# Kernel tuning notes

Hardware: AMD Instinct MI355X
Metric: run time of the kernel (lower is better)

Reference implementation:

```python
import jax, jax.numpy as jnp
import numpy as np

D_MODEL = 1024
NUM_HEADS = 16
HEAD_DIM = D_MODEL // NUM_HEADS
THETA = 10000.0
B, S = 2, 2048


def _apply_rope(t, cos, sin):
    # t: [B, H, S, hd]; cos/sin: [S, hd//2]
    te = t[..., 0::2]
    to = t[..., 1::2]
    re = te * cos - to * sin
    ro = te * sin + to * cos
    out = jnp.stack([re, ro], axis=-1)  # [B,H,S,hd//2,2]
    return out.reshape(t.shape)


def setup_inputs() -> dict:
    key = jax.random.key(0)
    kx, kq, kk, kv, ko = jax.random.split(key, 5)
    std = 2.0 / (2 * D_MODEL) ** 0.5
    def w(k):
        return jnp.clip(std * jax.random.normal(k, (D_MODEL, D_MODEL), jnp.float32), -3.0 * std, 3.0 * std)
    return {
        "x": jax.random.normal(kx, (B, S, D_MODEL), jnp.float32),
        "Wq": w(kq),
        "Wk": w(kk),
        "Wv": w(kv),
        "Wo": w(ko),
    }


def reference(x, Wq, Wk, Wv, Wo):
    Bv, Sv, _ = x.shape
    def proj(W):
        return jnp.einsum('bsd,ed->bse', x, W).reshape(Bv, Sv, NUM_HEADS, HEAD_DIM).transpose(0, 2, 1, 3)
    q, k, v = proj(Wq), proj(Wk), proj(Wv)

    pos = jnp.arange(Sv, dtype=jnp.float32)
    inv_freq = THETA ** (-jnp.arange(0, HEAD_DIM, 2, dtype=jnp.float32) / HEAD_DIM)
    ang = pos[:, None] * inv_freq[None, :]  # [S, hd//2]
    cos, sin = jnp.cos(ang), jnp.sin(ang)
    q = _apply_rope(q, cos, sin)
    k = _apply_rope(k, cos, sin)

    scale = 1.0 / jnp.sqrt(jnp.float32(HEAD_DIM))
    scores = jnp.einsum('bhqd,bhkd->bhqk', q.astype(jnp.float32), k.astype(jnp.float32)) * scale
    causal = jnp.tril(jnp.ones((Sv, Sv), dtype=bool))
    scores = jnp.where(causal[None, None], scores, -jnp.inf)
    attn = jax.nn.softmax(scores, axis=-1)
    out = jnp.einsum('bhqk,bhkd->bhqd', attn, v.astype(jnp.float32))
    out = out.transpose(0, 2, 1, 3).reshape(Bv, Sv, D_MODEL)
    return jnp.einsum('bsd,ed->bse', out, Wo)
```

## Files before the change

### kernel.cpp

```cpp
#include <hip/hip_runtime.h>
#include <hip/hip_bf16.h>
#include <stdint.h>

typedef __bf16 bf16x8 __attribute__((ext_vector_type(8)));
typedef float  f32x4  __attribute__((ext_vector_type(4)));

__device__ __forceinline__ float bf2f(unsigned short u) {
    union { float f; uint32_t i; } v; v.i = ((uint32_t)u) << 16; return v.f;
}
__device__ __forceinline__ unsigned short f2bf(float f) {
    union { float f; uint32_t i; } v; v.f = f;
    uint32_t r = v.i + 0x7FFF + ((v.i >> 16) & 1);
    return (unsigned short)(r >> 16);
}
__device__ __forceinline__ unsigned short f2bf_rz(float f) {
    union { float f; uint32_t i; } v; v.f = f;
    return (unsigned short)(v.i >> 16);
}

#define GLD_LDS(gptr, lptr) \
    __builtin_amdgcn_global_load_lds( \
        (const __attribute__((address_space(1))) void*)(gptr), \
        (__attribute__((address_space(3))) void*)(lptr), 16, 0, 0)

__global__ __launch_bounds__(256) void convert_inputs(
    const void* __restrict__ x,  const void* __restrict__ wq,
    const void* __restrict__ wk, const void* __restrict__ wv,
    const void* __restrict__ wo, unsigned short* __restrict__ dst,
    unsigned short* __restrict__ wob_dst, int* __restrict__ flag)
{
    __shared__ int cnt[256];
    const int tid = threadIdx.x;
    uint32_t u = ((const uint32_t*)x)[tid];
    int e = (u >> 7) & 0xFF;
    cnt[tid] = (e >= 100 && e <= 140) ? 1 : 0;
    __syncthreads();
    for (int s = 128; s > 0; s >>= 1) {
        if (tid < s) cnt[tid] += cnt[tid + s];
        __syncthreads();
    }
    const int isf32 = (cnt[0] >= 128) ? 0 : 1;
    if (blockIdx.x == 0 && tid == 0) flag[0] = isf32 ? 0 : 1;

    int c = blockIdx.x * 256 + tid;
    const void* src; size_t off; unsigned short* out;
    if (c < 524288)      { src = x;  off = (size_t)c * 8;            out = dst + (size_t)c * 8; }
    else if (c < 655360) { src = wq; off = (size_t)(c - 524288) * 8; out = dst + (size_t)c * 8; }
    else if (c < 786432) { src = wk; off = (size_t)(c - 655360) * 8; out = dst + (size_t)c * 8; }
    else if (c < 917504) { src = wv; off = (size_t)(c - 786432) * 8; out = dst + (size_t)c * 8; }
    else                 { src = wo; off = (size_t)(c - 917504) * 8; out = wob_dst + off; }
    unsigned short t[8];
    if (isf32) {
        const float* s = (const float*)src + off;
        float4 f0 = *(const float4*)s;
        float4 f1 = *(const float4*)(s + 4);
        t[0] = f2bf(f0.x); t[1] = f2bf(f0.y); t[2] = f2bf(f0.z); t[3] = f2bf(f0.w);
        t[4] = f2bf(f1.x); t[5] = f2bf(f1.y); t[6] = f2bf(f1.z); t[7] = f2bf(f1.w);
    } else {
        *(uint4*)t = *(const uint4*)((const unsigned short*)src + off);
    }
    *(uint4*)out = *(const uint4*)t;
}

__global__ __launch_bounds__(512, 2) void gemm_qkv_8ph(
    const unsigned short* __restrict__ A,
    const unsigned short* __restrict__ B0,
    const unsigned short* __restrict__ B1,
    const unsigned short* __restrict__ B2,
    unsigned short* __restrict__ O0,
    unsigned short* __restrict__ O1,
    unsigned short* __restrict__ O2)
{
    __shared__ __align__(16) unsigned short Asl[2][16384];
    __shared__ __align__(16) unsigned short Bsl[2][16384];

    const int tid  = threadIdx.x;
    const int lane = tid & 63;
    const int wid  = tid >> 6;
    const int wm   = wid >> 2;
    const int wn   = wid & 3;
    const int lr   = lane & 15;
    const int quad = lane >> 4;

    const int m0  = blockIdx.y * 256;
    const int n0g = blockIdx.x * 256;
    const int sel = n0g >> 10;
    const unsigned short* Bp = (sel == 0) ? B0 : ((sel == 1) ? B1 : B2);
    unsigned short* Optr     = (sel == 0) ? O0 : ((sel == 1) ? O1 : O2);
    const int n0  = n0g & 1023;

    const int sw0 = ((0 + quad) ^ (lr & 7)) * 8;
    const int sw1 = ((4 + quad) ^ (lr & 7)) * 8;

    f32x4 acc[2][4][2][2] = {};
    bf16x8 aF[4][2];
    bf16x8 bF[2][2];

#define STAGEA(T, H) do { \
    const int tA_ = (T); \
    _Pragma("unroll") \
    for (int p_ = 0; p_ < 2; ++p_) { \
        int c_   = p_ * 512 + tid; \
        int row_ = c_ >> 3; \
        int sc_  = ((c_ & 7) ^ (row_ & 7)) * 8; \
        GLD_LDS(&A[(size_t)(m0 + (H) * 128 + row_) * 1024 + tA_ * 64 + sc_], \
                &Asl[tA_ & 1][(H) * 8192 + c_ * 8]); \
    } } while (0)

#define STAGEB(T, H) do { \
    const int tB_ = (T); \
    _Pragma("unroll") \
    for (int p_ = 0; p_ < 2; ++p_) { \
        int c_   = p_ * 512 + tid; \
        int row_ = c_ >> 3; \
        int sc_  = ((c_ & 7) ^ (row_ & 7)) * 8; \
        GLD_LDS(&Bp[(size_t)(n0 + (H) * 128 + row_) * 1024 + tB_ * 64 + sc_], \
                &Bsl[tB_ & 1][(H) * 8192 + c_ * 8]); \
    } } while (0)

#define LOADA(BUF, QM) do { \
    _Pragma("unroll") \
    for (int fm_ = 0; fm_ < 4; ++fm_) { \
        const int row_ = (QM) * 128 + wm * 64 + fm_ * 16 + lr; \
        aF[fm_][0] = *(const bf16x8*)&Asl[BUF][row_ * 64 + sw0]; \
        aF[fm_][1] = *(const bf16x8*)&Asl[BUF][row_ * 64 + sw1]; \
    } } while (0)

#define LOADB(BUF, QN) do { \
    _Pragma("unroll") \
    for (int fn_ = 0; fn_ < 2; ++fn_) { \
        const int row_ = (QN) * 128 + wn * 32 + fn_ * 16 + lr; \
        bF[fn_][0] = *(const bf16x8*)&Bsl[BUF][row_ * 64 + sw0]; \
        bF[fn_][1] = *(const bf16x8*)&Bsl[BUF][row_ * 64 + sw1]; \
    } } while (0)

#define MFMA16(QM, QN) do { \
    __builtin_amdgcn_s_setprio(1); \
    _Pragma("unroll") \
    for (int fm_ = 0; fm_ < 4; ++fm_) { \
        _Pragma("unroll") \
        for (int fn_ = 0; fn_ < 2; ++fn_) { \
            acc[QM][fm_][QN][fn_] = __builtin_amdgcn_mfma_f32_16x16x32_bf16( \
                aF[fm_][0], bF[fn_][0], acc[QM][fm_][QN][fn_], 0, 0, 0); \
            acc[QM][fm_][QN][fn_] = __builtin_amdgcn_mfma_f32_16x16x32_bf16( \
                aF[fm_][1], bF[fn_][1], acc[QM][fm_][QN][fn_], 0, 0, 0); \
        } \
    } \
    __builtin_amdgcn_s_setprio(0); \
    } while (0)

#define BARRIER() __builtin_amdgcn_s_barrier()
#define LGKM0()   asm volatile("s_waitcnt lgkmcnt(0)" ::: "memory")

    STAGEB(0, 0);
    STAGEA(0, 1);
    STAGEA(0, 0);
    STAGEB(0, 1);
    STAGEB(1, 0);
    STAGEA(1, 1);
    asm volatile("s_waitcnt vmcnt(4)" ::: "memory");
    BARRIER();

    const int NT = 16;
#pragma unroll 2
    for (int t = 0; t < NT; ++t) {
        const int buf = t & 1;

        LOADA(buf, 0);
        LOADB(buf, 0);
        if (t + 1 < NT) STAGEA(t + 1, 0);
        BARRIER();
        LGKM0();
        MFMA16(0, 0);
        BARRIER();

        LOADA(buf, 1);
        if (t + 1 < NT) STAGEB(t + 1, 1);
        BARRIER();
        LGKM0();
        MFMA16(1, 0);
        BARRIER();

        LOADB(buf, 1);
        if (t + 2 < NT) STAGEB(t + 2, 0);
        BARRIER();
        LGKM0();
        MFMA16(1, 1);
        BARRIER();

        LOADA(buf, 0);
        if (t + 2 < NT) STAGEA(t + 2, 1);
        BARRIER();
        LGKM0();
        MFMA16(0, 1);
        if (t + 2 < NT) asm volatile("s_waitcnt vmcnt(4)" ::: "memory");
        else            asm volatile("s_waitcnt vmcnt(0)" ::: "memory");
        BARRIER();
    }

#pragma unroll
    for (int qm = 0; qm < 2; ++qm) {
#pragma unroll
        for (int fm = 0; fm < 4; ++fm) {
            const int mb = m0 + qm * 128 + wm * 64 + fm * 16 + quad * 4;
#pragma unroll
            for (int qn = 0; qn < 2; ++qn) {
#pragma unroll
                for (int fn = 0; fn < 2; ++fn) {
                    const int nl = n0 + qn * 128 + wn * 32 + fn * 16 + lr;
                    const int h = nl >> 6, d = nl & 63;
#pragma unroll
                    for (int r = 0; r < 4; ++r) {
                        const int m = mb + r;
                        const int b = m >> 11, s = m & 2047;
                        Optr[((size_t)(b * 16 + h) * 2048 + s) * 64 + d] =
                            f2bf(acc[qm][fm][qn][fn][r]);
                    }
                }
            }
        }
    }
#undef STAGEA
#undef STAGEB
#undef LOADA
#undef LOADB
#undef MFMA16
#undef BARRIER
#undef LGKM0
}

__global__ __launch_bounds__(256) void gemm_out(
    const unsigned short* __restrict__ P0,
    const unsigned short* __restrict__ P1,
    const float* __restrict__ Lsum,
    const unsigned short* __restrict__ B0,
    void* __restrict__ O,
    const int* __restrict__ flag)
{
    const int K = 1024;
    __shared__ __align__(16) unsigned short As[64 * 64];
    __shared__ __align__(16) unsigned short Bs[128 * 64];

    const int isf32 = (flag[0] == 0) ? 1 : 0;

    const int tid  = threadIdx.x;
    const int lane = tid & 63;
    const int wid  = tid >> 6;
    const int wm   = wid >> 1;
    const int wn   = wid & 1;
    const int lr   = lane & 15;
    const int quad = lane >> 4;
    const int q8   = quad * 8;

    const int m0 = blockIdx.y * 64;
    const int n0 = blockIdx.x * 128;

    f32x4 acc[2][4] = {};

    for (int kk = 0; kk < K; kk += 64) {
        __syncthreads();
        const int h = kk >> 6;
        for (int p = 0; p < 2; ++p) {
            int c   = p * 256 + tid;
            int row = c >> 3;
            int d0  = (c & 7) * 8;
            int m   = m0 + row;
            int b   = m >> 11, s = m & 2047;
            int li  = (b * 16 + h) * 2048 + s;
            float inv = 1.0f / (Lsum[li] + Lsum[65536 + li]);
            size_t addr = ((size_t)li) * 64 + d0;
            unsigned short a[8], bb[8], o[8];
            *(uint4*)a  = *(const uint4*)&P0[addr];
            *(uint4*)bb = *(const uint4*)&P1[addr];
            for (int j = 0; j < 8; ++j)
                o[j] = f2bf((bf2f(a[j]) + bf2f(bb[j])) * inv);
            *(uint4*)&As[c * 8] = *(const uint4*)o;
        }
        for (int p = 0; p < 4; ++p) {
            int c   = p * 256 + tid;
            int row = c >> 3;
            int c8  = (c & 7) * 8;
            GLD_LDS(&B0[(size_t)(n0 + row) * K + kk + c8], &Bs[c * 8]);
        }
        __syncthreads();

        for (int ks = 0; ks < 64; ks += 32) {
            bf16x8 af[2], bf[4];
            for (int t = 0; t < 2; ++t)
                af[t] = *(const bf16x8*)&As[(wm * 32 + t * 16 + lr) * 64 + ks + q8];
            for (int t = 0; t < 4; ++t)
                bf[t] = *(const bf16x8*)&Bs[(wn * 64 + t * 16 + lr) * 64 + ks + q8];
            for (int mt = 0; mt < 2; ++mt)
                for (int nt = 0; nt < 4; ++nt)
                    acc[mt][nt] = __builtin_amdgcn_mfma_f32_16x16x32_bf16(
                        af[mt], bf[nt], acc[mt][nt], 0, 0, 0);
        }
    }

    for (int mt = 0; mt < 2; ++mt) {
        for (int nt = 0; nt < 4; ++nt) {
            for (int r = 0; r < 4; ++r) {
                int m  = m0 + wm * 32 + mt * 16 + quad * 4 + r;
                int nl = n0 + wn * 64 + nt * 16 + lr;
                float val = acc[mt][nt][r];
                if (isf32) ((float*)O)[(size_t)m * 1024 + nl] = val;
                else ((unsigned short*)O)[(size_t)m * 1024 + nl] = f2bf(val);
            }
        }
    }
}

__global__ __launch_bounds__(256) void rope_transpose(
    unsigned short* __restrict__ Q, unsigned short* __restrict__ Kp,
    const unsigned short* __restrict__ V, unsigned short* __restrict__ Vt)
{
    __shared__ unsigned short T[64 * 65];
    const int tid = threadIdx.x;

    if (blockIdx.x < 4096) {
        const int CH = 32 * 2048 * 8;
        int idx = blockIdx.x * 256 + tid;
        bool isK = idx >= CH;
        int j = isK ? (idx - CH) : idx;
        unsigned short* p = isK ? Kp : Q;

        int c8   = j & 7;
        int srow = j >> 3;
        int s    = srow & 2047;
        int off  = srow * 64 + c8 * 8;

        uint4 raw = *(const uint4*)&p[off];
        unsigned short t[8];
        *(uint4*)t = raw;
        float sf = (float)s;
        float qs = isK ? 1.0f : 0.125f;
        for (int jj = 0; jj < 4; ++jj) {
            int i = c8 * 4 + jj;
            float inv = __expf(-0.2878231366f * (float)i);
            float ang = sf * inv;
            float sn = __sinf(ang);
            float cs = __cosf(ang);
            float e = bf2f(t[2 * jj]);
            float o = bf2f(t[2 * jj + 1]);
            t[2 * jj]     = f2bf((e * cs - o * sn) * qs);
            t[2 * jj + 1] = f2bf((e * sn + o * cs) * qs);
        }
        *(uint4*)&p[off] = *(const uint4*)t;
    } else {
        int bidx = blockIdx.x - 4096;
        const int s0 = (bidx & 31) * 64;
        const int bh = bidx >> 5;

        const unsigned short* src = V + ((size_t)bh * 2048 + s0) * 64;
        for (int p = 0; p < 2; ++p) {
            int c = p * 256 + tid;
            int s  = c >> 3;
            int d8 = (c & 7) * 8;
            uint4 raw = *(const uint4*)&src[s * 64 + d8];
            unsigned short t[8];
            *(uint4*)t = raw;
            for (int j = 0; j < 8; ++j) T[s * 65 + d8 + j] = t[j];
        }
        __syncthreads();
        unsigned short* dst = Vt + (size_t)bh * 64 * 2048 + s0;
        for (int p = 0; p < 2; ++p) {
            int c = p * 256 + tid;
            int d  = c >> 3;
            int s8 = (c & 7) * 8;
            unsigned short t[8];
            for (int j = 0; j < 8; ++j) t[j] = T[(s8 + j) * 65 + d];
            *(uint4*)&dst[(size_t)d * 2048 + s8] = *(const uint4*)t;
        }
    }
}

__global__ __launch_bounds__(256) void attn_kernel(
    const unsigned short* __restrict__ Q,
    const unsigned short* __restrict__ Kp,
    const unsigned short* __restrict__ Vt,
    unsigned short* __restrict__ P0,
    unsigned short* __restrict__ P1,
    float* __restrict__ Lsum)
{
    __shared__ __align__(16) unsigned short Ks[2][4096];
    __shared__ __align__(16) unsigned short Vs[2][4096];
    __shared__ __align__(16) unsigned short Ps[4096];

    const int tid  = threadIdx.x;
    const int lane = tid & 63;
    const int w    = tid >> 6;
    const int lr   = lane & 15;
    const int quad = lane >> 4;
    const int q8   = quad * 8;
    const int wps  = w * 1024;

    const int bh    = blockIdx.x;
    const int y     = blockIdx.y;
    const int split = y >> 4;
    const int yq    = y & 15;
    const int qb    = (yq < 8) ? yq : (23 - yq);
    const int q0    = qb * 128;
    const int kb0   = split ? (qb + 1) : 0;
    const int kb1   = split ? (2 * qb + 1) : qb;

    unsigned short* Pout = split ? P1 : P0;

    const unsigned short* KbBase = Kp + (size_t)bh * 2048 * 64;
    const unsigned short* VbBase = Vt + (size_t)bh * 131072;

    auto stage = [&](int kb, int buf) {
        const unsigned short* Kb = KbBase + kb * 64 * 64;
        const unsigned short* Vb = VbBase + kb * 64;
        for (int p = 0; p < 2; ++p) {
            int c    = p * 256 + tid;
            int f    = c >> 6, l = c & 63;
            int nt   = f >> 1, ks = f & 1;
            int lr_s = l & 15, qd = l >> 4;
            GLD_LDS(&Kb[(nt * 16 + lr_s) * 64 + ks * 32 + qd * 8], &Ks[buf][c * 8]);
            GLD_LDS(&Vb[(size_t)(nt * 16 + lr_s) * 2048 + ks * 32 + qd * 8], &Vs[buf][c * 8]);
        }
    };

    bf16x8 qa[2][2];
    for (int mt = 0; mt < 2; ++mt) {
        const unsigned short* Qw = Q + ((size_t)bh * 2048 + q0 + mt * 64 + w * 16 + lr) * 64;
        qa[mt][0] = *(const bf16x8*)&Qw[q8];
        qa[mt][1] = *(const bf16x8*)&Qw[32 + q8];
    }

    stage(kb0, 0);

    f32x4 oacc[2][4] = {};
    float lpart[2][4] = {};
    const int l8 = lane * 8;
    const int lr7 = lr & 7;
    const int lrh = lr >> 3;

    for (int kb = kb0; kb <= kb1; ++kb) {
        const int cur = (kb - kb0) & 1;
        __syncthreads();
        if (kb < kb1) stage(kb + 1, cur ^ 1);

        f32x4 sacc[2][4] = {};
        for (int nt = 0; nt < 4; ++nt) {
            bf16x8 kf0 = *(const bf16x8*)&Ks[cur][(nt * 2 + 0) * 512 + l8];
            bf16x8 kf1 = *(const bf16x8*)&Ks[cur][(nt * 2 + 1) * 512 + l8];
            for (int mt = 0; mt < 2; ++mt) {
                sacc[mt][nt] = __builtin_amdgcn_mfma_f32_16x16x32_bf16(qa[mt][0], kf0, sacc[mt][nt], 0, 0, 0);
                sacc[mt][nt] = __builtin_amdgcn_mfma_f32_16x16x32_bf16(qa[mt][1], kf1, sacc[mt][nt], 0, 0, 0);
            }
        }

        if (kb >= 2 * qb) {
            for (int mt = 0; mt < 2; ++mt) {
                int rowb = q0 + mt * 64 + w * 16 + quad * 4;
                for (int nt = 0; nt < 4; ++nt) {
                    int col = kb * 64 + nt * 16 + lr;
                    for (int r = 0; r < 4; ++r)
                        if (col > rowb + r) sacc[mt][nt][r] = -3.0e38f;
                }
            }
        }

        for (int mt = 0; mt < 2; ++mt) {
            for (int r = 0; r < 4; ++r) {
                for (int nt = 0; nt < 4; ++nt) {
                    float pv = __expf(sacc[mt][nt][r] - 16.0f);
                    lpart[mt][r] += pv;
                    int ks = nt >> 1;
                    int qr = (nt * 2 + lrh) & 3;
                    Ps[wps + ks * 512 + (qr * 16 + quad * 4 + r) * 8 + lr7] = f2bf_rz(pv);
                }
            }
            for (int ks = 0; ks < 2; ++ks) {
                bf16x8 pa = *(const bf16x8*)&Ps[wps + ks * 512 + l8];
                for (int nt = 0; nt < 4; ++nt) {
                    bf16x8 vf = *(const bf16x8*)&Vs[cur][(nt * 2 + ks) * 512 + l8];
                    oacc[mt][nt] = __builtin_amdgcn_mfma_f32_16x16x32_bf16(pa, vf, oacc[mt][nt], 0, 0, 0);
                }
            }
        }
    }

    for (int mt = 0; mt < 2; ++mt) {
        for (int r = 0; r < 4; ++r) {
            float l = lpart[mt][r];
            for (int off = 1; off < 16; off <<= 1)
                l += __shfl_xor(l, off, 64);
            int s = q0 + mt * 64 + w * 16 + quad * 4 + r;
            for (int nt = 0; nt < 4; ++nt)
                Pout[((size_t)bh * 2048 + s) * 64 + nt * 16 + lr] = f2bf_rz(oacc[mt][nt][r]);
            if (lr == 0) Lsum[split * 65536 + bh * 2048 + s] = l;
        }
    }
}

extern "C" void kernel_launch(void* const* d_in, const int* in_sizes, int n_in,
                              void* d_out, int out_size, void* d_ws, size_t ws_size,
                              hipStream_t stream)
{
    const void* x  = d_in[0];
    const void* Wq = d_in[1];
    const void* Wk = d_in[2];
    const void* Wv = d_in[3];
    const void* Wo = d_in[4];

    int* flag = (int*)d_ws;
    unsigned short* base = (unsigned short*)d_ws + 8;
    const size_t M1 = 1048576;
    unsigned short* xb  = base;
    unsigned short* wqb = base + 4 * M1;
    unsigned short* wkb = base + 5 * M1;
    unsigned short* wvb = base + 6 * M1;
    unsigned short* q   = base + 8 * M1;
    unsigned short* k   = base + 12 * M1;
    unsigned short* v   = base + 16 * M1;
    unsigned short* wob = base + 20 * M1;
    float*          Ls  = (float*)(base + 21 * M1);
    unsigned short* vt  = xb;
    unsigned short* P0  = v;
    unsigned short* P1  = wqb;

    convert_inputs<<<dim3(4096), 256, 0, stream>>>(x, Wq, Wk, Wv, Wo, base, wob, flag);
    gemm_qkv_8ph<<<dim3(12, 16), 512, 0, stream>>>(xb, wqb, wkb, wvb, q, k, v);
    rope_transpose<<<dim3(5120), 256, 0, stream>>>(q, k, v, vt);
    attn_kernel<<<dim3(32, 32), 256, 0, stream>>>(q, k, vt, P0, P1, Ls);
    gemm_out<<<dim3(8, 64), 256, 0, stream>>>(P0, P1, Ls, wob, d_out, flag);
}
```

Baseline: 215.2 us.

## Load K/V fragments directly from global memory, dropping LDS staging

```diff
diff --git a/kernel.cpp b/kernel.cpp
--- a/kernel.cpp
+++ b/kernel.cpp
@@ -382,9 +382,7 @@
     unsigned short* __restrict__ P1,
     float* __restrict__ Lsum)
 {
-    __shared__ __align__(16) unsigned short Ks[2][4096];
-    __shared__ __align__(16) unsigned short Vs[2][4096];
-    __shared__ __align__(16) unsigned short Ps[4096];
+    __shared__ __align__(16) unsigned short Ps[2][4096];
 
     const int tid  = threadIdx.x;
     const int lane = tid & 63;
@@ -405,21 +403,8 @@
 
     unsigned short* Pout = split ? P1 : P0;
 
-    const unsigned short* KbBase = Kp + (size_t)bh * 2048 * 64;
-    const unsigned short* VbBase = Vt + (size_t)bh * 131072;
-
-    auto stage = [&](int kb, int buf) {
-        const unsigned short* Kb = KbBase + kb * 64 * 64;
-        const unsigned short* Vb = VbBase + kb * 64;
-        for (int p = 0; p < 2; ++p) {
-            int c    = p * 256 + tid;
-            int f    = c >> 6, l = c & 63;
-            int nt   = f >> 1, ks = f & 1;
-            int lr_s = l & 15, qd = l >> 4;
-            GLD_LDS(&Kb[(nt * 16 + lr_s) * 64 + ks * 32 + qd * 8], &Ks[buf][c * 8]);
-            GLD_LDS(&Vb[(size_t)(nt * 16 + lr_s) * 2048 + ks * 32 + qd * 8], &Vs[buf][c * 8]);
-        }
-    };
+    const unsigned short* Kfrag = Kp + (size_t)bh * 131072 + lr * 64   + q8;
+    const unsigned short* Vfrag = Vt + (size_t)bh * 131072 + lr * 2048 + q8;
 
     bf16x8 qa[2][2];
     for (int mt = 0; mt < 2; ++mt) {
@@ -428,23 +413,21 @@
         qa[mt][1] = *(const bf16x8*)&Qw[32 + q8];
     }
 
-    stage(kb0, 0);
-
     f32x4 oacc[2][4] = {};
     float lpart[2][4] = {};
-    const int l8 = lane * 8;
+    const int l8  = lane * 8;
     const int lr7 = lr & 7;
     const int lrh = lr >> 3;
+    const float LOG2E = 1.4426950408889634f;
 
     for (int kb = kb0; kb <= kb1; ++kb) {
-        const int cur = (kb - kb0) & 1;
-        __syncthreads();
-        if (kb < kb1) stage(kb + 1, cur ^ 1);
-
         f32x4 sacc[2][4] = {};
+        const unsigned short* Kb = Kfrag + (size_t)kb * 4096;
+#pragma unroll
         for (int nt = 0; nt < 4; ++nt) {
-            bf16x8 kf0 = *(const bf16x8*)&Ks[cur][(nt * 2 + 0) * 512 + l8];
-            bf16x8 kf1 = *(const bf16x8*)&Ks[cur][(nt * 2 + 1) * 512 + l8];
+            bf16x8 kf0 = *(const bf16x8*)&Kb[nt * 1024];
+            bf16x8 kf1 = *(const bf16x8*)&Kb[nt * 1024 + 32];
+#pragma unroll
             for (int mt = 0; mt < 2; ++mt) {
                 sacc[mt][nt] = __builtin_amdgcn_mfma_f32_16x16x32_bf16(qa[mt][0], kf0, sacc[mt][nt], 0, 0, 0);
                 sacc[mt][nt] = __builtin_amdgcn_mfma_f32_16x16x32_bf16(qa[mt][1], kf1, sacc[mt][nt], 0, 0, 0);
@@ -452,32 +435,44 @@
         }
 
         if (kb >= 2 * qb) {
+#pragma unroll
             for (int mt = 0; mt < 2; ++mt) {
                 int rowb = q0 + mt * 64 + w * 16 + quad * 4;
+#pragma unroll
                 for (int nt = 0; nt < 4; ++nt) {
                     int col = kb * 64 + nt * 16 + lr;
+#pragma unroll
                     for (int r = 0; r < 4; ++r)
                         if (col > rowb + r) sacc[mt][nt][r] = -3.0e38f;
                 }
             }
         }
 
+#pragma unroll
         for (int mt = 0; mt < 2; ++mt) {
+#pragma unroll
             for (int r = 0; r < 4; ++r) {
+#pragma unroll
                 for (int nt = 0; nt < 4; ++nt) {
-                    float pv = __expf(sacc[mt][nt][r] - 16.0f);
+                    float pv = exp2f(fmaf(sacc[mt][nt][r], LOG2E, -23.083120654223414f));
                     lpart[mt][r] += pv;
                     int ks = nt >> 1;
                     int qr = (nt * 2 + lrh) & 3;
-                    Ps[wps + ks * 512 + (qr * 16 + quad * 4 + r) * 8 + lr7] = f2bf_rz(pv);
+                    Ps[mt][wps + ks * 512 + (qr * 16 + quad * 4 + r) * 8 + lr7] = f2bf_rz(pv);
                 }
             }
-            for (int ks = 0; ks < 2; ++ks) {
-                bf16x8 pa = *(const bf16x8*)&Ps[wps + ks * 512 + l8];
-                for (int nt = 0; nt < 4; ++nt) {
-                    bf16x8 vf = *(const bf16x8*)&Vs[cur][(nt * 2 + ks) * 512 + l8];
-                    oacc[mt][nt] = __builtin_amdgcn_mfma_f32_16x16x32_bf16(pa, vf, oacc[mt][nt], 0, 0, 0);
-                }
+        }
+
+        const unsigned short* Vb = Vfrag + kb * 64;
+#pragma unroll
+        for (int ks = 0; ks < 2; ++ks) {
+            bf16x8 pa0 = *(const bf16x8*)&Ps[0][wps + ks * 512 + l8];
+            bf16x8 pa1 = *(const bf16x8*)&Ps[1][wps + ks * 512 + l8];
+#pragma unroll
+            for (int nt = 0; nt < 4; ++nt) {
+                bf16x8 vf = *(const bf16x8*)&Vb[nt * 32768 + ks * 32];
+                oacc[0][nt] = __builtin_amdgcn_mfma_f32_16x16x32_bf16(pa0, vf, oacc[0][nt], 0, 0, 0);
+                oacc[1][nt] = __builtin_amdgcn_mfma_f32_16x16x32_bf16(pa1, vf, oacc[1][nt], 0, 0, 0);
             }
         }
     }
```

Measured after the change: 259.1 us. 20.4% more time.
